# Kernel optimization log

Hardware: AMD Instinct MI355X
Metric: run time of the kernel (lower is better)

## Reference

```python
import jax, jax.numpy as jnp
import numpy as np

N, E, D, R = 50000, 600000, 128, 500


def setup_inputs() -> dict:
    key = jax.random.key(0)
    ks = jax.random.split(key, 9)
    h = jax.random.normal(ks[0], (N, D), dtype=jnp.float32)
    norm = jax.random.uniform(ks[1], (N, 1), dtype=jnp.float32)
    emb_rel = jax.random.normal(ks[2], (R, D), dtype=jnp.float32)
    scale = 1.0 / np.sqrt(D)  # xavier-ish scale for DxD weights
    weight_neighbor = jax.random.normal(ks[3], (D, D), dtype=jnp.float32) * scale
    loop_weight = jax.random.normal(ks[4], (D, D), dtype=jnp.float32) * scale
    evolve_loop_weight = jax.random.normal(ks[5], (D, D), dtype=jnp.float32) * scale
    src = jax.random.randint(ks[6], (E,), 0, N, dtype=jnp.int32)
    dst = jax.random.randint(ks[7], (E,), 0, N, dtype=jnp.int32)
    etype = jax.random.randint(ks[8], (E,), 0, R, dtype=jnp.int32)
    return {
        "h": h, "norm": norm, "emb_rel": emb_rel,
        "weight_neighbor": weight_neighbor, "loop_weight": loop_weight,
        "evolve_loop_weight": evolve_loop_weight,
        "src": src, "dst": dst, "etype": etype,
    }


def reference(h, norm, emb_rel, weight_neighbor, loop_weight,
              evolve_loop_weight, src, dst, etype):
    # msg_func: gather src node features + relation embeddings, add, dense matmul
    msg = (h[src] + emb_rel[etype]) @ weight_neighbor        # [E, D]
    # update_all(fn.sum): scatter-sum messages into destination nodes
    agg = jax.ops.segment_sum(msg, dst, num_segments=N)       # [N, D]
    # apply_func: scale by per-node norm
    h_agg = agg * norm                                        # [N, D]
    # self-loop: nodes with in-degree > 0 use loop_weight, others evolve_loop_weight
    in_deg = jax.ops.segment_sum(jnp.ones((E,), dtype=jnp.float32), dst,
                                 num_segments=N)              # [N]
    loop_msg = jnp.where((in_deg > 0)[:, None],
                         h @ loop_weight,
                         h @ evolve_loop_weight)              # [N, D]
    node_repr = h_agg + loop_msg
    return jax.nn.relu(node_repr)
```

## Files before the change

### kernel.cpp

```cpp
#include <hip/hip_runtime.h>
#include <hip/hip_bf16.h>


#define DIM 128

typedef __attribute__((ext_vector_type(8))) short bf16x8_t;
typedef __attribute__((ext_vector_type(4))) float f32x4_t;

__device__ inline ushort f2bf(float f) {
    __hip_bfloat16 b = __float2bfloat16(f);
    return *reinterpret_cast<ushort*>(&b);
}
__device__ inline float bf2f(ushort u) {
    unsigned v = ((unsigned)u) << 16;
    return __uint_as_float(v);
}
__device__ inline uint4 cvt8(const float4& a, const float4& b) {
    uint4 o;
    o.x = f2bf(a.x) | ((unsigned)f2bf(a.y) << 16);
    o.y = f2bf(a.z) | ((unsigned)f2bf(a.w) << 16);
    o.z = f2bf(b.x) | ((unsigned)f2bf(b.y) << 16);
    o.w = f2bf(b.z) | ((unsigned)f2bf(b.w) << 16);
    return o;
}

__global__ __launch_bounds__(256) void init_kernel(
    const float4* __restrict__ h4, const float4* __restrict__ emb4,
    const float* __restrict__ Wn, const float* __restrict__ Wl,
    uint4* __restrict__ h8, uint4* __restrict__ emb8,
    ushort* __restrict__ Bpack, int* __restrict__ head,
    int* __restrict__ zcount, int nH8, int nE8, int N)
{
    int i = blockIdx.x * 256 + threadIdx.x;
    if (i < nH8) {
        h8[i] = cvt8(h4[2 * i], h4[2 * i + 1]);
        return;
    }
    int j = i - nH8;
    if (j < nE8) {
        emb8[j] = cvt8(emb4[2 * j], emb4[2 * j + 1]);
        return;
    }
    j -= nE8;
    if (j < 32768) {
        int jj   = j & 7;
        int lane = (j >> 3) & 63;
        int ks   = (j >> 9) & 7;
        int nt   = j >> 12;
        int k = ks * 32 + (lane >> 4) * 8 + jj;
        int n = nt * 16 + (lane & 15);
        float v = (k < DIM) ? Wn[k * DIM + n] : Wl[(k - DIM) * DIM + n];
        Bpack[j] = f2bf(v);
        return;
    }
    j -= 32768;
    if (j < N) { head[j] = -1; return; }
    if (j == N) *zcount = 0;
}

__global__ __launch_bounds__(256) void build_kernel(
    const int4* __restrict__ src4, const int4* __restrict__ dst4,
    const int4* __restrict__ et4, int* __restrict__ head,
    uint2* __restrict__ list, int E4,
    const int* __restrict__ src, const int* __restrict__ dst,
    const int* __restrict__ etype, int E)
{
    int i = blockIdx.x * 256 + threadIdx.x;
    if (i < E4) {
        int4 s = src4[i], d = dst4[i], t = et4[i];
        int e = 4 * i;
        int old;
        old = atomicExch(head + d.x, e + 0);
        list[e + 0] = make_uint2((unsigned)s.x | ((unsigned)t.x << 17), (unsigned)old);
        old = atomicExch(head + d.y, e + 1);
        list[e + 1] = make_uint2((unsigned)s.y | ((unsigned)t.y << 17), (unsigned)old);
        old = atomicExch(head + d.z, e + 2);
        list[e + 2] = make_uint2((unsigned)s.z | ((unsigned)t.z << 17), (unsigned)old);
        old = atomicExch(head + d.w, e + 3);
        list[e + 3] = make_uint2((unsigned)s.w | ((unsigned)t.w << 17), (unsigned)old);
    }
    if (i == 0)
        for (int e = E4 * 4; e < E; ++e) {
            int old = atomicExch(head + dst[e], e);
            list[e] = make_uint2((unsigned)src[e] | ((unsigned)etype[e] << 17),
                                 (unsigned)old);
        }
}

__device__ inline void addbf8(float* a, uint4 hv, uint4 rv) {
    a[0] += bf2f((ushort)(hv.x & 0xFFFF)) + bf2f((ushort)(rv.x & 0xFFFF));
    a[1] += bf2f((ushort)(hv.x >> 16))    + bf2f((ushort)(rv.x >> 16));
    a[2] += bf2f((ushort)(hv.y & 0xFFFF)) + bf2f((ushort)(rv.y & 0xFFFF));
    a[3] += bf2f((ushort)(hv.y >> 16))    + bf2f((ushort)(rv.y >> 16));
    a[4] += bf2f((ushort)(hv.z & 0xFFFF)) + bf2f((ushort)(rv.z & 0xFFFF));
    a[5] += bf2f((ushort)(hv.z >> 16))    + bf2f((ushort)(rv.z >> 16));
    a[6] += bf2f((ushort)(hv.w & 0xFFFF)) + bf2f((ushort)(rv.w & 0xFFFF));
    a[7] += bf2f((ushort)(hv.w >> 16))    + bf2f((ushort)(rv.w >> 16));
}

__global__ __launch_bounds__(256) void gather_kernel(
    const uint4* __restrict__ h8,
    const uint4* __restrict__ emb8,
    const float* __restrict__ norm,
    const int* __restrict__ head,
    const uint2* __restrict__ list,
    uint4* __restrict__ aggn8,
    int* __restrict__ zcount, int* __restrict__ zlist,
    int N)
{
    int n = blockIdx.x * 16 + (threadIdx.x >> 4);
    if (n >= N) return;
    int lane = threadIdx.x & 15;
    int cur = head[n];

    if (cur < 0) {
        if (lane == 0) {
            int p = atomicAdd(zcount, 1);
            zlist[p] = n;
        }
        aggn8[(size_t)n * 16 + lane] = make_uint4(0, 0, 0, 0);
        return;
    }

    float a[8] = {0.f, 0.f, 0.f, 0.f, 0.f, 0.f, 0.f, 0.f};
    while (cur >= 0) {
        uint2 v = list[cur];
        unsigned p = v.x;
        cur = (int)v.y;
        uint4 hv = h8[(size_t)(p & 0x1FFFF) * 16 + lane];
        uint4 rv = emb8[(size_t)(p >> 17) * 16 + lane];
        addbf8(a, hv, rv);
    }
    float nm = norm[n];
    uint4 o;
    o.x = f2bf(a[0] * nm) | ((unsigned)f2bf(a[1] * nm) << 16);
    o.y = f2bf(a[2] * nm) | ((unsigned)f2bf(a[3] * nm) << 16);
    o.z = f2bf(a[4] * nm) | ((unsigned)f2bf(a[5] * nm) << 16);
    o.w = f2bf(a[6] * nm) | ((unsigned)f2bf(a[7] * nm) << 16);
    aggn8[(size_t)n * 16 + lane] = o;
}

__global__ __launch_bounds__(256) void mfma_gemm_kernel(
    const ushort* __restrict__ aggn_bf,
    const ushort* __restrict__ h_bf,
    const ushort* __restrict__ Bpack,
    float* __restrict__ out,
    int nRowTiles, int halfWaves)
{
    int wave = threadIdx.x >> 6;
    int lane = threadIdx.x & 63;
    int wid  = blockIdx.x * 4 + wave;
    int ch   = wid & 1;
    int w    = wid >> 1;
    int m    = lane & 15;
    int quad = lane >> 4;

    bf16x8_t b[4][8];
    #pragma unroll
    for (int nt = 0; nt < 4; ++nt)
        #pragma unroll
        for (int ks = 0; ks < 8; ++ks)
            b[nt][ks] = *(const bf16x8_t*)(Bpack +
                (((size_t)(ch * 4 + nt) * 8 + ks) * 64 + lane) * 8);

    for (int rt = w; rt < nRowTiles; rt += halfWaves) {
        size_t rowOff = (size_t)(rt * 16 + m) * DIM + quad * 8;
        bf16x8_t a[8];
        #pragma unroll
        for (int ks = 0; ks < 4; ++ks) {
            a[ks]     = *(const bf16x8_t*)(aggn_bf + rowOff + ks * 32);
            a[ks + 4] = *(const bf16x8_t*)(h_bf   + rowOff + ks * 32);
        }
        f32x4_t acc[4];
        #pragma unroll
        for (int nt = 0; nt < 4; ++nt)
            #pragma unroll
            for (int r = 0; r < 4; ++r) acc[nt][r] = 0.f;

        #pragma unroll
        for (int ks = 0; ks < 8; ++ks)
            #pragma unroll
            for (int nt = 0; nt < 4; ++nt)
                acc[nt] = __builtin_amdgcn_mfma_f32_16x16x32_bf16(
                    a[ks], b[nt][ks], acc[nt], 0, 0, 0);

        int colBase = ch * 64 + m;
        int rowBase = rt * 16 + quad * 4;
        #pragma unroll
        for (int nt = 0; nt < 4; ++nt)
            #pragma unroll
            for (int r = 0; r < 4; ++r)
                out[(size_t)(rowBase + r) * DIM + colBase + nt * 16] =
                    fmaxf(acc[nt][r], 0.f);
    }
}

__global__ __launch_bounds__(128) void fixup_kernel(
    const float* __restrict__ h, const float* __restrict__ We,
    const int* __restrict__ zlist, const int* __restrict__ zcount,
    float* __restrict__ out)
{
    int cnt = *zcount;
    int c = threadIdx.x;
    for (int i = blockIdx.x; i < cnt; i += gridDim.x) {
        int n = zlist[i];
        float s = 0.f;
        for (int k = 0; k < DIM; ++k)
            s = fmaf(h[(size_t)n * DIM + k], We[(size_t)k * DIM + c], s);
        out[(size_t)n * DIM + c] = fmaxf(s, 0.f);
    }
}

extern "C" void kernel_launch(void* const* d_in, const int* in_sizes, int n_in,
                              void* d_out, int out_size, void* d_ws, size_t ws_size,
                              hipStream_t stream)
{
    const float* h    = (const float*)d_in[0];
    const float* norm = (const float*)d_in[1];
    const float* emb  = (const float*)d_in[2];
    const float* Wn   = (const float*)d_in[3];
    const float* Wl   = (const float*)d_in[4];
    const float* We   = (const float*)d_in[5];
    const int* src    = (const int*)d_in[6];
    const int* dst    = (const int*)d_in[7];
    const int* etype  = (const int*)d_in[8];

    const int N = in_sizes[1];
    const int E = in_sizes[6];
    const int R = in_sizes[2] / DIM;

    char* p = (char*)d_ws;
    ushort* h_bf    = (ushort*)p;  p += (size_t)N * DIM * 2;
    ushort* emb_bf  = (ushort*)p;  p += (size_t)R * DIM * 2;
    ushort* Bpack   = (ushort*)p;  p += 2 * DIM * DIM * 2;
    ushort* aggn_bf = (ushort*)p;  p += (size_t)N * DIM * 2;
    uint2*  list    = (uint2*)p;   p += (size_t)E * 8;
    int*    head    = (int*)p;     p += ((size_t)N * 4 + 15) & ~(size_t)15;
    int*    zcount  = (int*)p;     p += 16;
    int*    zlist   = (int*)p;

    const int nH8 = N * DIM / 8;
    const int nE8 = R * DIM / 8;
    const int initTotal = nH8 + nE8 + 32768 + N + 1;

    init_kernel<<<dim3((initTotal + 255) / 256), dim3(256), 0, stream>>>(
        (const float4*)h, (const float4*)emb, Wn, Wl,
        (uint4*)h_bf, (uint4*)emb_bf, Bpack, head, zcount, nH8, nE8, N);

    build_kernel<<<dim3((E / 4 + 255) / 256), dim3(256), 0, stream>>>(
        (const int4*)src, (const int4*)dst, (const int4*)etype,
        head, list, E / 4, src, dst, etype, E);

    gather_kernel<<<dim3((N + 15) / 16), dim3(256), 0, stream>>>(
        (const uint4*)h_bf, (const uint4*)emb_bf, norm, head, list,
        (uint4*)aggn_bf, zcount, zlist, N);

    const int nRowTiles = (N + 15) / 16;
    mfma_gemm_kernel<<<dim3(512), dim3(256), 0, stream>>>(
        aggn_bf, h_bf, Bpack, (float*)d_out, nRowTiles, 1024);

    fixup_kernel<<<dim3(2), dim3(128), 0, stream>>>(
        h, We, zlist, zcount, (float*)d_out);
}
```

Baseline: 174.9 us.

## Split per-node edge linked lists into four interleaved chains for parallel traversal

Each destination node now gets four list heads, and an edge goes into chain (edge index mod 4). The gather kernel loads all four heads as an int4 and walks the four chains together, issuing up to four independent list and feature loads per iteration. This is meant to cut the serial pointer-chasing latency that dominated the gather and to spread the build-time atomic exchanges over more addresses. In exchange the head array is four times larger, which needs more workspace and more init work, and the loop has more branch divergence.

Measured after the change: 176.8 us. Within noise of the previous version (+1.1%).

```diff
diff --git a/kernel.cpp b/kernel.cpp
--- a/kernel.cpp
+++ b/kernel.cpp
@@ -29,7 +29,7 @@
     const float* __restrict__ Wn, const float* __restrict__ Wl,
     uint4* __restrict__ h8, uint4* __restrict__ emb8,
     ushort* __restrict__ Bpack, int* __restrict__ head,
-    int* __restrict__ zcount, int nH8, int nE8, int N)
+    int* __restrict__ zcount, int nH8, int nE8, int headN)
 {
     int i = blockIdx.x * 256 + threadIdx.x;
     if (i < nH8) {
@@ -54,8 +54,8 @@
         return;
     }
     j -= 32768;
-    if (j < N) { head[j] = -1; return; }
-    if (j == N) *zcount = 0;
+    if (j < headN) { head[j] = -1; return; }
+    if (j == headN) *zcount = 0;
 }
 
 __global__ __launch_bounds__(256) void build_kernel(
@@ -70,18 +70,18 @@
         int4 s = src4[i], d = dst4[i], t = et4[i];
         int e = 4 * i;
         int old;
-        old = atomicExch(head + d.x, e + 0);
+        old = atomicExch(head + d.x * 4 + 0, e + 0);
         list[e + 0] = make_uint2((unsigned)s.x | ((unsigned)t.x << 17), (unsigned)old);
-        old = atomicExch(head + d.y, e + 1);
+        old = atomicExch(head + d.y * 4 + 1, e + 1);
         list[e + 1] = make_uint2((unsigned)s.y | ((unsigned)t.y << 17), (unsigned)old);
-        old = atomicExch(head + d.z, e + 2);
+        old = atomicExch(head + d.z * 4 + 2, e + 2);
         list[e + 2] = make_uint2((unsigned)s.z | ((unsigned)t.z << 17), (unsigned)old);
-        old = atomicExch(head + d.w, e + 3);
+        old = atomicExch(head + d.w * 4 + 3, e + 3);
         list[e + 3] = make_uint2((unsigned)s.w | ((unsigned)t.w << 17), (unsigned)old);
     }
     if (i == 0)
         for (int e = E4 * 4; e < E; ++e) {
-            int old = atomicExch(head + dst[e], e);
+            int old = atomicExch(head + dst[e] * 4 + (e & 3), e);
             list[e] = make_uint2((unsigned)src[e] | ((unsigned)etype[e] << 17),
                                  (unsigned)old);
         }
@@ -102,7 +102,7 @@
     const uint4* __restrict__ h8,
     const uint4* __restrict__ emb8,
     const float* __restrict__ norm,
-    const int* __restrict__ head,
+    const int4* __restrict__ head4,
     const uint2* __restrict__ list,
     uint4* __restrict__ aggn8,
     int* __restrict__ zcount, int* __restrict__ zlist,
@@ -111,9 +111,9 @@
     int n = blockIdx.x * 16 + (threadIdx.x >> 4);
     if (n >= N) return;
     int lane = threadIdx.x & 15;
-    int cur = head[n];
-
-    if (cur < 0) {
+    int4 c = head4[n];
+
+    if ((c.x & c.y & c.z & c.w) < 0) {
         if (lane == 0) {
             int p = atomicAdd(zcount, 1);
             zlist[p] = n;
@@ -122,16 +122,41 @@
         return;
     }
 
+    float nm = norm[n];
     float a[8] = {0.f, 0.f, 0.f, 0.f, 0.f, 0.f, 0.f, 0.f};
-    while (cur >= 0) {
-        uint2 v = list[cur];
-        unsigned p = v.x;
-        cur = (int)v.y;
-        uint4 hv = h8[(size_t)(p & 0x1FFFF) * 16 + lane];
-        uint4 rv = emb8[(size_t)(p >> 17) * 16 + lane];
-        addbf8(a, hv, rv);
-    }
-    float nm = norm[n];
+    do {
+        bool b0 = c.x >= 0, b1 = c.y >= 0, b2 = c.z >= 0, b3 = c.w >= 0;
+        uint2 v0, v1, v2, v3;
+        if (b0) v0 = list[c.x];
+        if (b1) v1 = list[c.y];
+        if (b2) v2 = list[c.z];
+        if (b3) v3 = list[c.w];
+        if (b0) {
+            uint4 hv = h8[(size_t)(v0.x & 0x1FFFF) * 16 + lane];
+            uint4 rv = emb8[(size_t)(v0.x >> 17) * 16 + lane];
+            addbf8(a, hv, rv);
+            c.x = (int)v0.y;
+        }
+        if (b1) {
+            uint4 hv = h8[(size_t)(v1.x & 0x1FFFF) * 16 + lane];
+            uint4 rv = emb8[(size_t)(v1.x >> 17) * 16 + lane];
+            addbf8(a, hv, rv);
+            c.y = (int)v1.y;
+        }
+        if (b2) {
+            uint4 hv = h8[(size_t)(v2.x & 0x1FFFF) * 16 + lane];
+            uint4 rv = emb8[(size_t)(v2.x >> 17) * 16 + lane];
+            addbf8(a, hv, rv);
+            c.z = (int)v2.y;
+        }
+        if (b3) {
+            uint4 hv = h8[(size_t)(v3.x & 0x1FFFF) * 16 + lane];
+            uint4 rv = emb8[(size_t)(v3.x >> 17) * 16 + lane];
+            addbf8(a, hv, rv);
+            c.w = (int)v3.y;
+        }
+    } while ((c.x & c.y & c.z & c.w) >= 0);
+
     uint4 o;
     o.x = f2bf(a[0] * nm) | ((unsigned)f2bf(a[1] * nm) << 16);
     o.y = f2bf(a[2] * nm) | ((unsigned)f2bf(a[3] * nm) << 16);
@@ -235,24 +260,25 @@
     ushort* Bpack   = (ushort*)p;  p += 2 * DIM * DIM * 2;
     ushort* aggn_bf = (ushort*)p;  p += (size_t)N * DIM * 2;
     uint2*  list    = (uint2*)p;   p += (size_t)E * 8;
-    int*    head    = (int*)p;     p += ((size_t)N * 4 + 15) & ~(size_t)15;
+    int*    head    = (int*)p;     p += ((size_t)N * 16 + 15) & ~(size_t)15;
     int*    zcount  = (int*)p;     p += 16;
     int*    zlist   = (int*)p;
 
     const int nH8 = N * DIM / 8;
     const int nE8 = R * DIM / 8;
-    const int initTotal = nH8 + nE8 + 32768 + N + 1;
+    const int headN = 4 * N;
+    const int initTotal = nH8 + nE8 + 32768 + headN + 1;
 
     init_kernel<<<dim3((initTotal + 255) / 256), dim3(256), 0, stream>>>(
         (const float4*)h, (const float4*)emb, Wn, Wl,
-        (uint4*)h_bf, (uint4*)emb_bf, Bpack, head, zcount, nH8, nE8, N);
+        (uint4*)h_bf, (uint4*)emb_bf, Bpack, head, zcount, nH8, nE8, headN);
 
     build_kernel<<<dim3((E / 4 + 255) / 256), dim3(256), 0, stream>>>(
         (const int4*)src, (const int4*)dst, (const int4*)etype,
         head, list, E / 4, src, dst, etype, E);
 
     gather_kernel<<<dim3((N + 15) / 16), dim3(256), 0, stream>>>(
-        (const uint4*)h_bf, (const uint4*)emb_bf, norm, head, list,
+        (const uint4*)h_bf, (const uint4*)emb_bf, norm, (const int4*)head, list,
         (uint4*)aggn_bf, zcount, zlist, N);
 
     const int nRowTiles = (N + 15) / 16;
```
